# Performance work log

Hardware: AMD Instinct MI355X
Metric: run time of the kernel (lower is better)

## Reference

```python
import jax, jax.numpy as jnp
import numpy as np

HIDDEN = 2048
NUM_HEADS = 32
HEAD_DIM = 64
NUM_KV = 8
GROUP = NUM_HEADS // NUM_KV
SCALE = HEAD_DIM ** -0.5
ROPE_BASE = 10000.0


def apply_rope(t):
    # t: [B, H, S, D]; standard half-split rotary embedding
    S, D = t.shape[-2], t.shape[-1]
    inv_freq = 1.0 / (ROPE_BASE ** (jnp.arange(0, D, 2, dtype=jnp.float32) / D))  # [D/2]
    ang = jnp.arange(S, dtype=jnp.float32)[:, None] * inv_freq[None, :]           # [S, D/2]
    cos, sin = jnp.cos(ang), jnp.sin(ang)
    x1, x2 = t[..., : D // 2], t[..., D // 2 :]
    return jnp.concatenate([x1 * cos - x2 * sin, x2 * cos + x1 * sin], axis=-1)


def setup_inputs() -> dict:
    key = jax.random.key(0)
    ks = jax.random.split(key, 10)
    B, S = 2, 2048
    s_in = HIDDEN ** -0.5
    s_o = (NUM_HEADS * HEAD_DIM) ** -0.5
    return {
        "x": jax.random.normal(ks[0], (B, S, HIDDEN), jnp.float32),
        "Wq": jax.random.normal(ks[1], (NUM_HEADS * HEAD_DIM, HIDDEN), jnp.float32) * s_in,
        "bq": jnp.zeros((NUM_HEADS * HEAD_DIM,), jnp.float32),
        "Wk": jax.random.normal(ks[2], (NUM_KV * HEAD_DIM, HIDDEN), jnp.float32) * s_in,
        "bk": jnp.zeros((NUM_KV * HEAD_DIM,), jnp.float32),
        "Wv": jax.random.normal(ks[3], (NUM_KV * HEAD_DIM, HIDDEN), jnp.float32) * s_in,
        "bv": jnp.zeros((NUM_KV * HEAD_DIM,), jnp.float32),
        "Wo": jax.random.normal(ks[4], (HIDDEN, NUM_HEADS * HEAD_DIM), jnp.float32) * s_o,
        "bo": jnp.zeros((HIDDEN,), jnp.float32),
        "key_weights": jax.random.normal(ks[5], (NUM_HEADS,), jnp.float32),
    }


def reference(x, Wq, bq, Wk, bk, Wv, bv, Wo, bo, key_weights):
    B, S, _ = x.shape
    q = (x @ Wq.T + bq).reshape(B, S, NUM_HEADS, HEAD_DIM).transpose(0, 2, 1, 3)
    k = (x @ Wk.T + bk).reshape(B, S, NUM_KV, HEAD_DIM).transpose(0, 2, 1, 3)
    v = (x @ Wv.T + bv).reshape(B, S, NUM_KV, HEAD_DIM).transpose(0, 2, 1, 3)
    q = apply_rope(q)
    k = apply_rope(k)
    # group queries per KV head: [B, kv, g, S, D]
    qg = q.reshape(B, NUM_KV, GROUP, S, HEAD_DIM)
    scores = jnp.einsum("bkgsd,bktd->bkgst", qg, k) * SCALE
    scores = scores * key_weights.reshape(1, NUM_KV, GROUP, 1, 1)
    causal = jnp.tril(jnp.ones((S, S), bool))
    scores = jnp.where(causal, scores, -jnp.inf)
    a = jax.nn.softmax(scores, axis=-1)
    o = jnp.einsum("bkgst,bktd->bkgsd", a, v)  # [B, kv, g, S, D]
    o = o.reshape(B, NUM_HEADS, S, HEAD_DIM).transpose(0, 2, 1, 3).reshape(B, S, NUM_HEADS * HEAD_DIM)
    return o @ Wo.T + bo
```

## Files before the change

kernel.cpp:

```cpp
#include <hip/hip_runtime.h>
#include <stdint.h>

#define S_LEN 2048
#define HID   2048
#define NH    32
#define NKV   8
#define HD    64
#define BATCH 2
#define NROWS (BATCH * S_LEN)
#define QKVN  (NH*HD + 2*NKV*HD)

typedef unsigned short u16;
typedef __bf16 bf16_t;
typedef bf16_t bf16x8 __attribute__((ext_vector_type(8)));
typedef float  f32x4  __attribute__((ext_vector_type(4)));
typedef float  f32x16 __attribute__((ext_vector_type(16)));
typedef u16    u16x8  __attribute__((ext_vector_type(8)));

#define LOG2E 1.4426950408889634f

__device__ __forceinline__ u16 f2bf(float f) {
    union { float f; uint32_t u; } v; v.f = f;
    uint32_t u = v.u;
    return (u16)((u + 0x7fffu + ((u >> 16) & 1u)) >> 16);
}

__device__ __forceinline__ unsigned cvtpk(float a, float b) {
    unsigned r;
    asm("v_cvt_pk_bf16_f32 %0, %1, %2" : "=v"(r) : "v"(a), "v"(b));
    return r;
}

__device__ __forceinline__ void plswap(unsigned &a, unsigned &b) {
    asm volatile("v_permlane32_swap_b32 %0, %1" : "+v"(a), "+v"(b));
}

__device__ __forceinline__ void llds16(const void* g, void* l) {
    __builtin_amdgcn_global_load_lds(
        (const __attribute__((address_space(1))) void*)g,
        (__attribute__((address_space(3))) void*)l,
        16, 0, 0);
}

__device__ __forceinline__ unsigned swz(unsigned row) {
    return ((row ^ (row >> 2)) & 3u) << 4;
}

#define LGKM0() do { asm volatile("s_waitcnt lgkmcnt(0)" ::: "memory"); \
                     __builtin_amdgcn_sched_barrier(0); } while (0)
#define BAR()   __builtin_amdgcn_s_barrier()

#define CBAR(N) do { \
    asm volatile("s_waitcnt vmcnt(" #N ")" ::: "memory"); \
    __builtin_amdgcn_s_barrier(); \
    __builtin_amdgcn_sched_barrier(0); \
} while (0)

#define CVT_GROUPS 2359296
__global__ void prep_all(const float* __restrict__ x, const float* __restrict__ wq,
                         const float* __restrict__ wk, const float* __restrict__ wv,
                         const float* __restrict__ wo,
                         const float* __restrict__ bq, const float* __restrict__ bk,
                         const float* __restrict__ bv,
                         u16* __restrict__ xb, u16* __restrict__ wqkvb, u16* __restrict__ wob,
                         float* __restrict__ rtab, float* __restrict__ bqkv) {
    int e = blockIdx.x * 256 + threadIdx.x;
    if (e < CVT_GROUPS) {
        const float* s; u16* d; int o;
        if (e < 1048576)      { s = x;  d = xb;                 o = e; }
        else if (e < 1572864) { s = wq; d = wqkvb;              o = e - 1048576; }
        else if (e < 1703936) { s = wk; d = wqkvb + 2048*2048;  o = e - 1572864; }
        else if (e < 1835008) { s = wv; d = wqkvb + 2560*2048;  o = e - 1703936; }
        else                  { s = wo; d = wob;                o = e - 1835008; }
        const float4* sp = (const float4*)s;
        float4 a = sp[2*(size_t)o], b = sp[2*(size_t)o + 1];
        u16x8 r;
        r[0]=f2bf(a.x); r[1]=f2bf(a.y); r[2]=f2bf(a.z); r[3]=f2bf(a.w);
        r[4]=f2bf(b.x); r[5]=f2bf(b.y); r[6]=f2bf(b.z); r[7]=f2bf(b.w);
        *(u16x8*)(d + 8*(size_t)o) = r;
    } else if (e < CVT_GROUPS + 65536) {
        int idx = e - CVT_GROUPS;
        int i = idx & 31, s = idx >> 5;
        float invf = exp2f(-(float)i * (13.287712379549449f / 32.0f));
        float ang = (float)s * invf;
        float sn, cs;
        sincosf(ang, &sn, &cs);
        rtab[idx] = cs;
        rtab[S_LEN*32 + idx] = sn;
    } else if (e < CVT_GROUPS + 65536 + QKVN) {
        int i = e - CVT_GROUPS - 65536;
        bqkv[i] = (i < 2048) ? bq[i] : (i < 2560 ? bk[i - 2048] : bv[i - 2560]);
    }
}


__global__ __launch_bounds__(256, 2) void gemm_qkv(
    const u16* __restrict__ A, const u16* __restrict__ Bw,
    const float* __restrict__ bias, const float* __restrict__ rtab,
    const float* __restrict__ kw,
    u16* __restrict__ qpk, u16* __restrict__ kpk, u16* __restrict__ vlin)
{
    const int M = NROWS, N = QKVN, K = HID;
    const int nbn = N >> 8;
    const int nwg = (M >> 7) * nbn;
    int wg = blockIdx.x;
    wg = (wg & 7) * (nwg >> 3) + (wg >> 3);
    const int bm = wg / nbn, bn = wg % nbn;
    const int brow = bm << 7, bcol = bn << 8;

    __shared__ u16 sbuf[3][12288];

    const int t = threadIdx.x;
    const int lane = t & 63, wid = t >> 6;
    const int wr = wid >> 1, wn = wid & 1;
    const int lr = lane & 15, lhi = lane >> 4;

    auto stageA = [&](int kt, int bi) {
        const int k0 = kt << 5;
        #pragma unroll
        for (int i = 0; i < 2; ++i) {
            const unsigned off = ((unsigned)t << 4) + ((unsigned)i << 12);
            const unsigned row = off >> 6;
            const unsigned scb = (off & 63) ^ swz(row);
            llds16(A + (size_t)(brow + row) * K + (k0 + (scb >> 1)), &sbuf[bi][0] + (off >> 1));
        }
        {
            const unsigned off = ((unsigned)t << 4);
            const unsigned row = off >> 6;
            const unsigned scb = (off & 63) ^ swz(row);
            llds16(Bw + (size_t)(bcol + row) * K + (k0 + (scb >> 1)), &sbuf[bi][4096] + (off >> 1));
        }
    };
    auto stageB = [&](int kt, int bi) {
        const int k0 = kt << 5;
        #pragma unroll
        for (int i = 1; i < 4; ++i) {
            const unsigned off = ((unsigned)t << 4) + ((unsigned)i << 12);
            const unsigned row = off >> 6;
            const unsigned scb = (off & 63) ^ swz(row);
            llds16(Bw + (size_t)(bcol + row) * K + (k0 + (scb >> 1)), &sbuf[bi][4096] + (off >> 1));
        }
    };

    f32x4 acc[4][8] = {};
    const int nk = K >> 5;

    stageA(0, 0); stageB(0, 0);
    stageA(1, 1); stageB(1, 1);
    asm volatile("s_waitcnt vmcnt(6)" ::: "memory");
    BAR();

    int cur = 0, st2 = 2;
    for (int kt = 0; kt < nk; ++kt) {
        const char* sA = (const char*)&sbuf[cur][0];
        const char* sB = (const char*)&sbuf[cur][4096];
        bf16x8 af[4], bfv[8];
        #pragma unroll
        for (int m = 0; m < 4; ++m) {
            const unsigned row = wr*64 + m*16 + lr;
            af[m] = *(const bf16x8*)(sA + row*64 + ((unsigned)(lhi*16) ^ swz(row)));
        }
        #pragma unroll
        for (int n = 0; n < 4; ++n) {
            const unsigned row = wn*128 + n*16 + lr;
            bfv[n] = *(const bf16x8*)(sB + row*64 + ((unsigned)(lhi*16) ^ swz(row)));
        }
        if (kt + 2 < nk) stageA(kt + 2, st2);
        BAR();
        LGKM0();
        __builtin_amdgcn_s_setprio(1);
        #pragma unroll
        for (int m = 0; m < 4; ++m)
            #pragma unroll
            for (int n = 0; n < 4; ++n)
                acc[m][n] = __builtin_amdgcn_mfma_f32_16x16x32_bf16(af[m], bfv[n], acc[m][n], 0, 0, 0);
        __builtin_amdgcn_s_setprio(0);
        BAR();
        #pragma unroll
        for (int n = 4; n < 8; ++n) {
            const unsigned row = wn*128 + n*16 + lr;
            bfv[n] = *(const bf16x8*)(sB + row*64 + ((unsigned)(lhi*16) ^ swz(row)));
        }
        if (kt + 2 < nk) stageB(kt + 2, st2);
        BAR();
        LGKM0();
        __builtin_amdgcn_s_setprio(1);
        #pragma unroll
        for (int m = 0; m < 4; ++m)
            #pragma unroll
            for (int n = 4; n < 8; ++n)
                acc[m][n] = __builtin_amdgcn_mfma_f32_16x16x32_bf16(af[m], bfv[n], acc[m][n], 0, 0, 0);
        __builtin_amdgcn_s_setprio(0);
        if (kt + 2 < nk) {
            asm volatile("s_waitcnt vmcnt(6)" ::: "memory");
            BAR();
        } else if (kt + 1 < nk) {
            asm volatile("s_waitcnt vmcnt(0)" ::: "memory");
            BAR();
        }
        cur = (cur == 2) ? 0 : cur + 1;
        st2 = (st2 == 2) ? 0 : st2 + 1;
    }

    const int rowb = brow + wr*64;
    #pragma unroll
    for (int hg = 0; hg < 2; ++hg) {
        const int c64 = bcol + wn*128 + hg*64;
        const int hb  = c64 >> 6;
        if (hb < 40) {
            const bool isQ = hb < 32;
            const float sc = isQ ? (0.125f * LOG2E * kw[hb]) : 1.0f;
            u16* dst = isQ ? qpk : kpk;
            const int nheads = isQ ? 32 : 8;
            const int hloc = isQ ? hb : (hb - 32);
            #pragma unroll
            for (int m = 0; m < 4; ++m) {
                #pragma unroll
                for (int nn = 0; nn < 2; ++nn) {
                    const int n = 4*hg + nn;
                    const int i = nn*16 + lr;
                    const float b1 = bias[c64 + i];
                    const float b2 = bias[c64 + i + 32];
                    #pragma unroll
                    for (int j = 0; j < 4; ++j) {
                        const int row = rowb + m*16 + lhi*4 + j;
                        const int s = row & (S_LEN - 1);
                        const int bb = row >> 11;
                        const float x1 = acc[m][n][j] + b1;
                        const float x2 = acc[m][n+2][j] + b2;
                        const float cs = rtab[s*32 + i];
                        const float sn = rtab[S_LEN*32 + s*32 + i];
                        const size_t base = ((size_t)(bb*nheads + hloc)) * (S_LEN*64) + (size_t)s*64;
                        dst[base + i]      = f2bf((x1*cs - x2*sn) * sc);
                        dst[base + i + 32] = f2bf((x2*cs + x1*sn) * sc);
                    }
                }
            }
        } else {
            #pragma unroll
            for (int m = 0; m < 4; ++m) {
                #pragma unroll
                for (int nn = 0; nn < 4; ++nn) {
                    const int col = c64 + nn*16 + lr;
                    const float bv = bias[col];
                    #pragma unroll
                    for (int j = 0; j < 4; ++j) {
                        const int row = rowb + m*16 + lhi*4 + j;
                        vlin[(size_t)row * 512 + (col - 2560)] = f2bf(acc[m][nn + 4*hg][j] + bv);
                    }
                }
            }
        }
    }
}

__global__ __launch_bounds__(256, 2) void gemm_bt(
    const u16* __restrict__ A, const u16* __restrict__ Bw,
    const float* __restrict__ bias, float* __restrict__ C,
    int M, int N, int K)
{
    const int nbn = N >> 8;
    const int nwg = (M >> 7) * nbn;
    int wg = blockIdx.x;
    wg = (wg & 7) * (nwg >> 3) + (wg >> 3);
    const int bm = wg / nbn, bn = wg % nbn;
    const int brow = bm << 7, bcol = bn << 8;

    __shared__ u16 sbuf[3][12288];

    const int t = threadIdx.x;
    const int lane = t & 63, wid = t >> 6;
    const int wr = wid >> 1, wn = wid & 1;
    const int lr = lane & 15, lhi = lane >> 4;

    auto stageA = [&](int kt, int bi) {
        const int k0 = kt << 5;
        #pragma unroll
        for (int i = 0; i < 2; ++i) {
            const unsigned off = ((unsigned)t << 4) + ((unsigned)i << 12);
            const unsigned row = off >> 6;
            const unsigned scb = (off & 63) ^ swz(row);
            llds16(A + (size_t)(brow + row) * K + (k0 + (scb >> 1)), &sbuf[bi][0] + (off >> 1));
        }
        {
            const unsigned off = ((unsigned)t << 4);
            const unsigned row = off >> 6;
            const unsigned scb = (off & 63) ^ swz(row);
            llds16(Bw + (size_t)(bcol + row) * K + (k0 + (scb >> 1)), &sbuf[bi][4096] + (off >> 1));
        }
    };
    auto stageB = [&](int kt, int bi) {
        const int k0 = kt << 5;
        #pragma unroll
        for (int i = 1; i < 4; ++i) {
            const unsigned off = ((unsigned)t << 4) + ((unsigned)i << 12);
            const unsigned row = off >> 6;
            const unsigned scb = (off & 63) ^ swz(row);
            llds16(Bw + (size_t)(bcol + row) * K + (k0 + (scb >> 1)), &sbuf[bi][4096] + (off >> 1));
        }
    };

    f32x4 acc[4][8] = {};
    const int nk = K >> 5;

    stageA(0, 0); stageB(0, 0);
    stageA(1, 1); stageB(1, 1);
    asm volatile("s_waitcnt vmcnt(6)" ::: "memory");
    BAR();

    int cur = 0, st2 = 2;
    for (int kt = 0; kt < nk; ++kt) {
        const char* sA = (const char*)&sbuf[cur][0];
        const char* sB = (const char*)&sbuf[cur][4096];
        bf16x8 af[4], bfv[8];
        #pragma unroll
        for (int m = 0; m < 4; ++m) {
            const unsigned row = wr*64 + m*16 + lr;
            af[m] = *(const bf16x8*)(sA + row*64 + ((unsigned)(lhi*16) ^ swz(row)));
        }
        #pragma unroll
        for (int n = 0; n < 4; ++n) {
            const unsigned row = wn*128 + n*16 + lr;
            bfv[n] = *(const bf16x8*)(sB + row*64 + ((unsigned)(lhi*16) ^ swz(row)));
        }
        if (kt + 2 < nk) stageA(kt + 2, st2);
        BAR();
        LGKM0();
        __builtin_amdgcn_s_setprio(1);
        #pragma unroll
        for (int m = 0; m < 4; ++m)
            #pragma unroll
            for (int n = 0; n < 4; ++n)
                acc[m][n] = __builtin_amdgcn_mfma_f32_16x16x32_bf16(af[m], bfv[n], acc[m][n], 0, 0, 0);
        __builtin_amdgcn_s_setprio(0);
        BAR();
        #pragma unroll
        for (int n = 4; n < 8; ++n) {
            const unsigned row = wn*128 + n*16 + lr;
            bfv[n] = *(const bf16x8*)(sB + row*64 + ((unsigned)(lhi*16) ^ swz(row)));
        }
        if (kt + 2 < nk) stageB(kt + 2, st2);
        BAR();
        LGKM0();
        __builtin_amdgcn_s_setprio(1);
        #pragma unroll
        for (int m = 0; m < 4; ++m)
            #pragma unroll
            for (int n = 4; n < 8; ++n)
                acc[m][n] = __builtin_amdgcn_mfma_f32_16x16x32_bf16(af[m], bfv[n], acc[m][n], 0, 0, 0);
        __builtin_amdgcn_s_setprio(0);
        if (kt + 2 < nk) {
            asm volatile("s_waitcnt vmcnt(6)" ::: "memory");
            BAR();
        } else if (kt + 1 < nk) {
            asm volatile("s_waitcnt vmcnt(0)" ::: "memory");
            BAR();
        }
        cur = (cur == 2) ? 0 : cur + 1;
        st2 = (st2 == 2) ? 0 : st2 + 1;
    }

    #pragma unroll
    for (int m = 0; m < 4; ++m) {
        #pragma unroll
        for (int n = 0; n < 8; ++n) {
            const int col = bcol + wn*128 + n*16 + lr;
            const float bv = bias[col];
            #pragma unroll
            for (int j = 0; j < 4; ++j) {
                const int row = brow + wr*64 + m*16 + lhi*4 + j;
                C[(size_t)row * N + col] = acc[m][n][j] + bv;
            }
        }
    }
}

__global__ void pack_vt(const u16* __restrict__ vlin, u16* __restrict__ vtb) {
    __shared__ u16 tile[64][67];
    const int st = blockIdx.x;
    const int bk = blockIdx.y;
    const int t = threadIdx.x;
    const int b = bk >> 3, kvh = bk & 7;
    const int r = t >> 2, cg = (t & 3) << 4;
    const u16* src = vlin + ((size_t)(b*S_LEN + st*64 + r)) * 512 + kvh*64 + cg;
    #pragma unroll
    for (int j = 0; j < 16; ++j) tile[r][cg + j] = src[j];
    __syncthreads();
    const int d = t >> 2, sg = (t & 3) << 4;
    u16* dst = vtb + ((size_t)(bk*64 + d)) * S_LEN + st*64 + sg;
    #pragma unroll
    for (int j = 0; j < 16; ++j) dst[j] = tile[sg + j][d];
}

__global__ __launch_bounds__(512, 4) void attn_fwd(
    const u16* __restrict__ Q,
    const u16* __restrict__ Kk,
    const u16* __restrict__ Vt,
    u16* __restrict__ O)
{
    __shared__ u16 sK[3][64 * 64];
    __shared__ u16 sV[3][64 * 64];

    const int t = threadIdx.x;
    const int lane = t & 63, wid = t >> 6;
    const int hi = lane >> 5, lq = lane & 31;
    const int bid = blockIdx.x;
    const int qb = (bid < 256) ? (7 - (bid >> 6)) : ((bid >> 6) - 4);
    const int bh = bid & 63;
    const int b = bh >> 5, h = bh & 31;
    const int kvh = h >> 2;

    const u16* Kp = Kk + ((size_t)(b*NKV + kvh)) * (S_LEN * 64);
    const u16* Vp = Vt + ((size_t)(b*NKV + kvh)) * (64 * S_LEN);

    const int q0w = qb*256 + wid*32;
    const int qg  = q0w + lq;

    const u16* Qrow = Q + (((size_t)bh) * S_LEN + qg) * 64 + 8*hi;
    bf16x8 qf[4];
    #pragma unroll
    for (int kd = 0; kd < 4; ++kd)
        qf[kd] = *(const bf16x8*)(Qrow + 16*kd);

    f32x16 accO0 = {}, accO1 = {};
    float m_run = 0.f, l_run = 0.f;

    const int ntB = 4*qb + 4;
    const int tmax_w = (q0w + 31) >> 6;

    auto stageKV = [&](int kt, int bi) {
        const int kv = kt << 6;
        const unsigned row = t >> 3, cb = (t & 7) << 4;
        const unsigned scb = cb ^ ((row & 7) << 4);
        llds16(Kp + (size_t)(kv + row) * 64 + (scb >> 1), &sK[bi][0] + t*8);
        llds16(Vp + (size_t)row * S_LEN + kv + (scb >> 1), &sV[bi][0] + t*8);
    };

    stageKV(0, 0);
    stageKV(1, 1);
    int cur = 0, st2 = 2;

    for (int tt = 0; tt < ntB; ++tt) {
        if (tt < ntB - 1) CBAR(2); else CBAR(0);
        if (tt + 2 < ntB) stageKV(tt + 2, st2);
        if (tt <= tmax_w) {
            const int kv0 = tt * 64;
            const float nm = -m_run;
            f32x16 s0, s1;
            #pragma unroll
            for (int r = 0; r < 16; ++r) { s0[r] = nm; s1[r] = nm; }
            __builtin_amdgcn_s_setprio(1);
            #pragma unroll
            for (int kd = 0; kd < 4; ++kd) {
                const unsigned bc = ((unsigned)(32*kd + 16*hi)) ^ ((lq & 7) << 4);
                bf16x8 k0 = *(const bf16x8*)((const char*)&sK[cur][0] + lq*128 + bc);
                bf16x8 k1 = *(const bf16x8*)((const char*)&sK[cur][0] + (32 + lq)*128 + bc);
                s0 = __builtin_amdgcn_mfma_f32_32x32x16_bf16(k0, qf[kd], s0, 0, 0, 0);
                s1 = __builtin_amdgcn_mfma_f32_32x32x16_bf16(k1, qf[kd], s1, 0, 0, 0);
            }
            __builtin_amdgcn_s_setprio(0);
            if (kv0 + 63 > q0w) {
                #pragma unroll
                for (int r = 0; r < 16; ++r) {
                    const int kvg = kv0 + (r & 3) + 8*(r >> 2) + 4*hi;
                    if (kvg > qg)      s0[r] = -INFINITY;
                    if (kvg + 32 > qg) s1[r] = -INFINITY;
                }
            }
            float mx[8];
            #pragma unroll
            for (int r = 0; r < 8; ++r)
                mx[r] = fmaxf(fmaxf(s0[r], s0[r+8]), fmaxf(s1[r], s1[r+8]));
            float tm = fmaxf(fmaxf(fmaxf(mx[0], mx[1]), fmaxf(mx[2], mx[3])),
                             fmaxf(fmaxf(mx[4], mx[5]), fmaxf(mx[6], mx[7])));
            tm = fmaxf(tm, __shfl_xor(tm, 32));
            if (!__all(tm <= 8.0f)) {
                const float dd = fmaxf(tm, 0.f);
                const float al = __builtin_amdgcn_exp2f(-dd);
                m_run += dd;
                l_run *= al;
                #pragma unroll
                for (int r = 0; r < 16; ++r) { accO0[r] *= al; accO1[r] *= al; }
                #pragma unroll
                for (int r = 0; r < 16; ++r) { s0[r] -= dd; s1[r] -= dd; }
            }
            #pragma unroll
            for (int r = 0; r < 16; ++r) {
                s0[r] = __builtin_amdgcn_exp2f(s0[r]);
                s1[r] = __builtin_amdgcn_exp2f(s1[r]);
            }
            float sm[8];
            #pragma unroll
            for (int r = 0; r < 8; ++r)
                sm[r] = (s0[r] + s0[r+8]) + (s1[r] + s1[r+8]);
            float rs = ((sm[0]+sm[1]) + (sm[2]+sm[3])) + ((sm[4]+sm[5]) + (sm[6]+sm[7]));
            rs += __shfl_xor(rs, 32);
            l_run += rs;

            #pragma unroll
            for (int ks = 0; ks < 4; ++ks) {
                const f32x16& e = (ks & 2) ? s1 : s0;
                const int rb = (ks & 1) * 8;
                unsigned x0 = cvtpk(e[rb + 0], e[rb + 1]);
                unsigned x1 = cvtpk(e[rb + 2], e[rb + 3]);
                unsigned y0 = cvtpk(e[rb + 4], e[rb + 5]);
                unsigned y1 = cvtpk(e[rb + 6], e[rb + 7]);
                plswap(x0, y0);
                plswap(x1, y1);
                union { unsigned u[4]; bf16x8 v; } pb;
                pb.u[0] = x0; pb.u[1] = x1; pb.u[2] = y0; pb.u[3] = y1;
                const unsigned bc = ((unsigned)(32*ks + 16*hi)) ^ ((lq & 7) << 4);
                bf16x8 v0 = *(const bf16x8*)((const char*)&sV[cur][0] + lq*128 + bc);
                bf16x8 v1 = *(const bf16x8*)((const char*)&sV[cur][0] + (32 + lq)*128 + bc);
                __builtin_amdgcn_s_setprio(1);
                accO0 = __builtin_amdgcn_mfma_f32_32x32x16_bf16(v0, pb.v, accO0, 0, 0, 0);
                accO1 = __builtin_amdgcn_mfma_f32_32x32x16_bf16(v1, pb.v, accO1, 0, 0, 0);
                __builtin_amdgcn_s_setprio(0);
            }
        }
        cur = (cur == 2) ? 0 : cur + 1;
        st2 = (st2 == 2) ? 0 : st2 + 1;
    }

    const float inv = 1.0f / l_run;
    u16* orow = O + (((size_t)(b * S_LEN) + q0w + lq)) * (NH*HD) + h*64;
    #pragma unroll
    for (int g = 0; g < 4; ++g) {
        uint2 w0, w1;
        w0.x = cvtpk(accO0[4*g + 0] * inv, accO0[4*g + 1] * inv);
        w0.y = cvtpk(accO0[4*g + 2] * inv, accO0[4*g + 3] * inv);
        *(uint2*)(orow + 8*g + 4*hi) = w0;
        w1.x = cvtpk(accO1[4*g + 0] * inv, accO1[4*g + 1] * inv);
        w1.y = cvtpk(accO1[4*g + 2] * inv, accO1[4*g + 3] * inv);
        *(uint2*)(orow + 32 + 8*g + 4*hi) = w1;
    }
}

extern "C" void kernel_launch(void* const* d_in, const int* in_sizes, int n_in,
                              void* d_out, int out_size, void* d_ws, size_t ws_size,
                              hipStream_t stream) {
    const float* x  = (const float*)d_in[0];
    const float* Wq = (const float*)d_in[1];
    const float* bq = (const float*)d_in[2];
    const float* Wk = (const float*)d_in[3];
    const float* bk = (const float*)d_in[4];
    const float* Wv = (const float*)d_in[5];
    const float* bv = (const float*)d_in[6];
    const float* Wo = (const float*)d_in[7];
    const float* bo = (const float*)d_in[8];
    const float* kw = (const float*)d_in[9];

    uint8_t* ws = (uint8_t*)d_ws;
    u16*   xb    = (u16*)(ws);
    u16*   wqkvb = (u16*)(ws + 16777216);
    u16*   wob   = (u16*)(ws + 29360128);
    u16*   qpk   = (u16*)(ws + 37748736);
    u16*   kpk   = (u16*)(ws + 54525952);
    u16*   vlin  = (u16*)(ws + 58720256);
    u16*   vtb   = (u16*)(ws + 62914560);
    u16*   ob    = (u16*)(ws + 67108864);
    float* bqkv  = (float*)(ws + 83886080);
    float* rtab  = (float*)(ws + 83898368);

    prep_all<<<9484, 256, 0, stream>>>(x, Wq, Wk, Wv, Wo, bq, bk, bv,
                                       xb, wqkvb, wob, rtab, bqkv);

    gemm_qkv<<<384, 256, 0, stream>>>(xb, wqkvb, bqkv, rtab, kw, qpk, kpk, vlin);

    pack_vt<<<dim3(32, 16), 256, 0, stream>>>(vlin, vtb);

    attn_fwd<<<dim3(512), dim3(512), 0, stream>>>(qpk, kpk, vtb, ob);

    gemm_bt<<<256, 256, 0, stream>>>(ob, wob, bo, (float*)d_out, NROWS, HID, HID);

    (void)in_sizes; (void)n_in; (void)out_size; (void)ws_size;
}
```

Measured before the change: 184.5 us.

## Retile QKV GEMM to 256x256 tiles with 8 waves and BK=64 double buffering

After: 183.6 us (median of 2 runs). Within noise of the previous version (-0.5%).

```diff
diff --git a/kernel.cpp b/kernel.cpp
--- a/kernel.cpp
+++ b/kernel.cpp
@@ -93,163 +93,174 @@
     }
 }
 
-
-__global__ __launch_bounds__(256, 2) void gemm_qkv(
+__global__ __launch_bounds__(512, 2) void gemm_qkv(
     const u16* __restrict__ A, const u16* __restrict__ Bw,
     const float* __restrict__ bias, const float* __restrict__ rtab,
     const float* __restrict__ kw,
     u16* __restrict__ qpk, u16* __restrict__ kpk, u16* __restrict__ vlin)
 {
-    const int M = NROWS, N = QKVN, K = HID;
-    const int nbn = N >> 8;
-    const int nwg = (M >> 7) * nbn;
+    const int K = HID;
+    const int nbn = QKVN >> 8;
+    const int nwg = (NROWS >> 8) * nbn;
     int wg = blockIdx.x;
     wg = (wg & 7) * (nwg >> 3) + (wg >> 3);
     const int bm = wg / nbn, bn = wg % nbn;
-    const int brow = bm << 7, bcol = bn << 8;
-
-    __shared__ u16 sbuf[3][12288];
+    const int brow = bm << 8, bcol = bn << 8;
+
+    __shared__ u16 lds[2][32768];
 
     const int t = threadIdx.x;
     const int lane = t & 63, wid = t >> 6;
-    const int wr = wid >> 1, wn = wid & 1;
+    const int wm = wid >> 2, wn = wid & 3;
     const int lr = lane & 15, lhi = lane >> 4;
 
-    auto stageA = [&](int kt, int bi) {
-        const int k0 = kt << 5;
+    auto stgA = [&](int b, int mh, int kt) {
+        const int k0 = kt << 6;
         #pragma unroll
         for (int i = 0; i < 2; ++i) {
-            const unsigned off = ((unsigned)t << 4) + ((unsigned)i << 12);
-            const unsigned row = off >> 6;
-            const unsigned scb = (off & 63) ^ swz(row);
-            llds16(A + (size_t)(brow + row) * K + (k0 + (scb >> 1)), &sbuf[bi][0] + (off >> 1));
-        }
-        {
-            const unsigned off = ((unsigned)t << 4);
-            const unsigned row = off >> 6;
-            const unsigned scb = (off & 63) ^ swz(row);
-            llds16(Bw + (size_t)(bcol + row) * K + (k0 + (scb >> 1)), &sbuf[bi][4096] + (off >> 1));
-        }
-    };
-    auto stageB = [&](int kt, int bi) {
-        const int k0 = kt << 5;
-        #pragma unroll
-        for (int i = 1; i < 4; ++i) {
-            const unsigned off = ((unsigned)t << 4) + ((unsigned)i << 12);
-            const unsigned row = off >> 6;
-            const unsigned scb = (off & 63) ^ swz(row);
-            llds16(Bw + (size_t)(bcol + row) * K + (k0 + (scb >> 1)), &sbuf[bi][4096] + (off >> 1));
-        }
-    };
-
-    f32x4 acc[4][8] = {};
-    const int nk = K >> 5;
-
-    stageA(0, 0); stageB(0, 0);
-    stageA(1, 1); stageB(1, 1);
-    asm volatile("s_waitcnt vmcnt(6)" ::: "memory");
+            const unsigned row = (unsigned)(i*128 + mh*64) + (t >> 3);
+            const unsigned cb  = (t & 7) << 4;
+            const unsigned scb = cb ^ ((row & 7) << 4);
+            llds16(A + (size_t)(brow + row) * K + (k0 + (scb >> 1)),
+                   &lds[b][0] + (((row << 7) + cb) >> 1));
+        }
+    };
+    auto stgB = [&](int b, int nh, int kt) {
+        const int k0 = kt << 6;
+        #pragma unroll
+        for (int i = 0; i < 2; ++i) {
+            const unsigned ru  = (unsigned)(i*64) + (t >> 3);
+            const unsigned row = (ru >> 5)*64 + nh*32 + (ru & 31);
+            const unsigned cb  = (t & 7) << 4;
+            const unsigned scb = cb ^ ((row & 7) << 4);
+            llds16(Bw + (size_t)(bcol + row) * K + (k0 + (scb >> 1)),
+                   &lds[b][16384] + (((row << 7) + cb) >> 1));
+        }
+    };
+
+    f32x4 acc[8][4] = {};
+    bf16x8 af[4][2], bfv[2][2];
+
+    auto rdA = [&](int b, int mh) {
+        const char* base = (const char*)&lds[b][0];
+        #pragma unroll
+        for (int m = 0; m < 4; ++m)
+            #pragma unroll
+            for (int ks = 0; ks < 2; ++ks) {
+                const unsigned row = wm*128 + mh*64 + m*16 + lr;
+                af[m][ks] = *(const bf16x8*)(base + (row << 7) +
+                    (((unsigned)(ks*64 + lhi*16)) ^ ((row & 7) << 4)));
+            }
+    };
+    auto rdB = [&](int b, int nh) {
+        const char* base = (const char*)&lds[b][16384];
+        #pragma unroll
+        for (int n = 0; n < 2; ++n)
+            #pragma unroll
+            for (int ks = 0; ks < 2; ++ks) {
+                const unsigned row = wn*64 + nh*32 + n*16 + lr;
+                bfv[n][ks] = *(const bf16x8*)(base + (row << 7) +
+                    (((unsigned)(ks*64 + lhi*16)) ^ ((row & 7) << 4)));
+            }
+    };
+
+#define MFMA16(MH, NH) do { \
+    __builtin_amdgcn_s_setprio(1); \
+    _Pragma("unroll") \
+    for (int m = 0; m < 4; ++m) \
+        _Pragma("unroll") \
+        for (int n = 0; n < 2; ++n) \
+            _Pragma("unroll") \
+            for (int ks = 0; ks < 2; ++ks) \
+                acc[(MH)*4+m][(NH)*2+n] = __builtin_amdgcn_mfma_f32_16x16x32_bf16( \
+                    af[m][ks], bfv[n][ks], acc[(MH)*4+m][(NH)*2+n], 0, 0, 0); \
+    __builtin_amdgcn_s_setprio(0); \
+} while (0)
+
+    const int nkt = K >> 6;
+    stgA(0, 0, 0); stgA(0, 1, 0); stgB(0, 0, 0); stgB(0, 1, 0);
+    stgA(1, 0, 1); stgB(1, 0, 1);
+    asm volatile("s_waitcnt vmcnt(4)" ::: "memory");
     BAR();
 
-    int cur = 0, st2 = 2;
-    for (int kt = 0; kt < nk; ++kt) {
-        const char* sA = (const char*)&sbuf[cur][0];
-        const char* sB = (const char*)&sbuf[cur][4096];
-        bf16x8 af[4], bfv[8];
-        #pragma unroll
-        for (int m = 0; m < 4; ++m) {
-            const unsigned row = wr*64 + m*16 + lr;
-            af[m] = *(const bf16x8*)(sA + row*64 + ((unsigned)(lhi*16) ^ swz(row)));
-        }
-        #pragma unroll
-        for (int n = 0; n < 4; ++n) {
-            const unsigned row = wn*128 + n*16 + lr;
-            bfv[n] = *(const bf16x8*)(sB + row*64 + ((unsigned)(lhi*16) ^ swz(row)));
-        }
-        if (kt + 2 < nk) stageA(kt + 2, st2);
+    for (int it = 0; it < nkt/2; ++it) {
+        const int kt0 = 2*it, kt1 = 2*it + 1;
+        const bool s02 = (kt0 + 2 < nkt), s12 = (kt1 + 2 < nkt);
+        rdA(0, 0); rdB(0, 0);
+        stgA(1, 1, kt1);
+        BAR(); LGKM0(); MFMA16(0, 0); BAR();
+        rdB(0, 1);
+        stgB(1, 1, kt1);
+        BAR(); LGKM0(); MFMA16(0, 1); BAR();
+        rdA(0, 1); rdB(0, 0);
+        if (s02) stgA(0, 0, kt0 + 2);
+        BAR(); LGKM0(); MFMA16(1, 0); BAR();
+        rdB(0, 1);
+        if (s02) stgB(0, 0, kt0 + 2);
+        BAR(); LGKM0(); MFMA16(1, 1);
+        if (s02) { asm volatile("s_waitcnt vmcnt(4)" ::: "memory"); }
+        else     { asm volatile("s_waitcnt vmcnt(0)" ::: "memory"); }
         BAR();
-        LGKM0();
-        __builtin_amdgcn_s_setprio(1);
-        #pragma unroll
-        for (int m = 0; m < 4; ++m)
-            #pragma unroll
-            for (int n = 0; n < 4; ++n)
-                acc[m][n] = __builtin_amdgcn_mfma_f32_16x16x32_bf16(af[m], bfv[n], acc[m][n], 0, 0, 0);
-        __builtin_amdgcn_s_setprio(0);
+        rdA(1, 0); rdB(1, 0);
+        if (s02) stgA(0, 1, kt0 + 2);
+        BAR(); LGKM0(); MFMA16(0, 0); BAR();
+        rdB(1, 1);
+        if (s02) stgB(0, 1, kt0 + 2);
+        BAR(); LGKM0(); MFMA16(0, 1); BAR();
+        rdA(1, 1); rdB(1, 0);
+        if (s12) stgA(1, 0, kt1 + 2);
+        BAR(); LGKM0(); MFMA16(1, 0); BAR();
+        rdB(1, 1);
+        if (s12) stgB(1, 0, kt1 + 2);
+        BAR(); LGKM0(); MFMA16(1, 1);
+        asm volatile("s_waitcnt vmcnt(4)" ::: "memory");
         BAR();
-        #pragma unroll
-        for (int n = 4; n < 8; ++n) {
-            const unsigned row = wn*128 + n*16 + lr;
-            bfv[n] = *(const bf16x8*)(sB + row*64 + ((unsigned)(lhi*16) ^ swz(row)));
-        }
-        if (kt + 2 < nk) stageB(kt + 2, st2);
-        BAR();
-        LGKM0();
-        __builtin_amdgcn_s_setprio(1);
-        #pragma unroll
-        for (int m = 0; m < 4; ++m)
-            #pragma unroll
-            for (int n = 4; n < 8; ++n)
-                acc[m][n] = __builtin_amdgcn_mfma_f32_16x16x32_bf16(af[m], bfv[n], acc[m][n], 0, 0, 0);
-        __builtin_amdgcn_s_setprio(0);
-        if (kt + 2 < nk) {
-            asm volatile("s_waitcnt vmcnt(6)" ::: "memory");
-            BAR();
-        } else if (kt + 1 < nk) {
-            asm volatile("s_waitcnt vmcnt(0)" ::: "memory");
-            BAR();
-        }
-        cur = (cur == 2) ? 0 : cur + 1;
-        st2 = (st2 == 2) ? 0 : st2 + 1;
-    }
-
-    const int rowb = brow + wr*64;
-    #pragma unroll
-    for (int hg = 0; hg < 2; ++hg) {
-        const int c64 = bcol + wn*128 + hg*64;
-        const int hb  = c64 >> 6;
-        if (hb < 40) {
-            const bool isQ = hb < 32;
-            const float sc = isQ ? (0.125f * LOG2E * kw[hb]) : 1.0f;
-            u16* dst = isQ ? qpk : kpk;
-            const int nheads = isQ ? 32 : 8;
-            const int hloc = isQ ? hb : (hb - 32);
-            #pragma unroll
-            for (int m = 0; m < 4; ++m) {
+    }
+#undef MFMA16
+
+    const int rowb = brow + wm*128;
+    const int c64 = bcol + wn*64;
+    const int hb  = c64 >> 6;
+    if (hb < 40) {
+        const bool isQ = hb < 32;
+        const float sc = isQ ? (0.125f * LOG2E * kw[hb]) : 1.0f;
+        u16* dst = isQ ? qpk : kpk;
+        const int nheads = isQ ? 32 : 8;
+        const int hloc = isQ ? hb : (hb - 32);
+        #pragma unroll
+        for (int nn = 0; nn < 2; ++nn) {
+            const int i = nn*16 + lr;
+            const float b1 = bias[c64 + i];
+            const float b2 = bias[c64 + i + 32];
+            #pragma unroll
+            for (int mf = 0; mf < 8; ++mf) {
                 #pragma unroll
-                for (int nn = 0; nn < 2; ++nn) {
-                    const int n = 4*hg + nn;
-                    const int i = nn*16 + lr;
-                    const float b1 = bias[c64 + i];
-                    const float b2 = bias[c64 + i + 32];
-                    #pragma unroll
-                    for (int j = 0; j < 4; ++j) {
-                        const int row = rowb + m*16 + lhi*4 + j;
-                        const int s = row & (S_LEN - 1);
-                        const int bb = row >> 11;
-                        const float x1 = acc[m][n][j] + b1;
-                        const float x2 = acc[m][n+2][j] + b2;
-                        const float cs = rtab[s*32 + i];
-                        const float sn = rtab[S_LEN*32 + s*32 + i];
-                        const size_t base = ((size_t)(bb*nheads + hloc)) * (S_LEN*64) + (size_t)s*64;
-                        dst[base + i]      = f2bf((x1*cs - x2*sn) * sc);
-                        dst[base + i + 32] = f2bf((x2*cs + x1*sn) * sc);
-                    }
+                for (int j = 0; j < 4; ++j) {
+                    const int row = rowb + mf*16 + lhi*4 + j;
+                    const int s = row & (S_LEN - 1);
+                    const int bb = row >> 11;
+                    const float x1 = acc[mf][nn][j] + b1;
+                    const float x2 = acc[mf][nn+2][j] + b2;
+                    const float cs = rtab[s*32 + i];
+                    const float sn = rtab[S_LEN*32 + s*32 + i];
+                    const size_t base = ((size_t)(bb*nheads + hloc)) * (S_LEN*64) + (size_t)s*64;
+                    dst[base + i]      = f2bf((x1*cs - x2*sn) * sc);
+                    dst[base + i + 32] = f2bf((x2*cs + x1*sn) * sc);
                 }
             }
-        } else {
-            #pragma unroll
-            for (int m = 0; m < 4; ++m) {
+        }
+    } else {
+        #pragma unroll
+        for (int nn = 0; nn < 4; ++nn) {
+            const int col = c64 + nn*16 + lr;
+            const float bv = bias[col];
+            #pragma unroll
+            for (int mf = 0; mf < 8; ++mf)
                 #pragma unroll
-                for (int nn = 0; nn < 4; ++nn) {
-                    const int col = c64 + nn*16 + lr;
-                    const float bv = bias[col];
-                    #pragma unroll
-                    for (int j = 0; j < 4; ++j) {
-                        const int row = rowb + m*16 + lhi*4 + j;
-                        vlin[(size_t)row * 512 + (col - 2560)] = f2bf(acc[m][nn + 4*hg][j] + bv);
-                    }
+                for (int j = 0; j < 4; ++j) {
+                    const int row = rowb + mf*16 + lhi*4 + j;
+                    vlin[(size_t)row * 512 + (col - 2560)] = f2bf(acc[mf][nn][j] + bv);
                 }
-            }
         }
     }
 }
@@ -565,7 +576,7 @@
     prep_all<<<9484, 256, 0, stream>>>(x, Wq, Wk, Wv, Wo, bq, bk, bv,
                                        xb, wqkvb, wob, rtab, bqkv);
 
-    gemm_qkv<<<384, 256, 0, stream>>>(xb, wqkvb, bqkv, rtab, kw, qpk, kpk, vlin);
+    gemm_qkv<<<192, 512, 0, stream>>>(xb, wqkvb, bqkv, rtab, kw, qpk, kpk, vlin);
 
     pack_vt<<<dim3(32, 16), 256, 0, stream>>>(vlin, vtb);
 
```
